# Kernel optimization log

Measured on AMD Instinct MI355X. Metric: run time of the kernel, lower is better.

The kernel has to match this reference:

```python
import jax, jax.numpy as jnp
import numpy as np
from jax import lax

NUM_GROUPS = 1024
GROUP_SIZE = 32
INIT_DIST = 1e10  # matches torch's 10000000000.0 init


def setup_inputs() -> dict:
    key = jax.random.key(0)
    k1, k2 = jax.random.split(key)
    x = jax.random.normal(k1, (1, 65536, 3), dtype=jnp.float32)
    features = jax.random.normal(k2, (1, 65536, 64), dtype=jnp.float32)
    return {"x": x, "features": features}


def _fps(xyz, npoint):
    # xyz: [B, N, 3] -> centers: [1, npoint, 3] (original code assumes B==1)
    B, N, _ = xyz.shape
    init_dist = jnp.full((B, N), INIT_DIST, dtype=xyz.dtype)
    init_far = jnp.zeros((B,), dtype=jnp.int32)  # deterministic start (torch uses randint)

    def step(carry, _):
        distance, farthest = carry
        centroid = jnp.take_along_axis(xyz, farthest[:, None, None], axis=1)  # [B,1,3]
        dist = jnp.sum((xyz - centroid) ** 2, axis=-1)  # [B,N]
        distance = jnp.minimum(distance, dist)
        new_far = jnp.argmax(distance, axis=-1).astype(jnp.int32)
        return (distance, new_far), farthest

    _, centroids = lax.scan(step, (init_dist, init_far), None, length=npoint)
    centroids = centroids.T  # [B, npoint]
    # original: fps_data = xyz[0, fps_idx].unsqueeze(0)  (B==1 assumption)
    return xyz[0, centroids[0]][None]  # [1, npoint, 3]


def _square_distance(src, dst):
    # src: [B,G,3], dst: [B,N,3] -> [B,G,N]
    d = -2.0 * jnp.einsum("bgc,bnc->bgn", src, dst)
    d += jnp.sum(src ** 2, -1)[:, :, None]
    d += jnp.sum(dst ** 2, -1)[:, None, :]
    return d


def reference(x, features):
    centers = _fps(x, NUM_GROUPS)                 # [1,G,3]
    distances = _square_distance(centers, x)      # [1,G,N]
    _, nb_idx = lax.top_k(-distances, GROUP_SIZE)  # smallest-k -> [1,G,M]
    F = features.shape[-1]
    flat_feat = features.reshape(-1, F)
    neighbors = flat_feat[nb_idx.reshape(-1)].reshape(1, -1, GROUP_SIZE, F)
    nearest_center_idx = jnp.argmin(distances, axis=1)  # [1,N]
    return neighbors, nearest_center_idx
```

## Files before the change

kernel.cpp:

```cpp
#include <hip/hip_runtime.h>
#include <stdint.h>

#define N_PTS   65536
#define N_GRP   1024
#define K_NB    32
#define F_DIM   64

#define FPS_BLOCKS  16
#define FPS_THREADS 512
#define FPS_TT (FPS_BLOCKS*FPS_THREADS)
#define FPS_P  (N_PTS / FPS_TT)

__device__ __forceinline__ unsigned long long packMaxKey(float v, unsigned int idx) {
  return ((unsigned long long)__float_as_uint(v) << 32) | (0xFFFFFFFFu - idx);
}
__device__ __forceinline__ unsigned long long packMinKey(float v, unsigned int idx) {
  unsigned int b = __float_as_uint(v);
  b = (b & 0x80000000u) ? ~b : (b | 0x80000000u);
  return ((unsigned long long)b << 32) | idx;
}
__device__ __forceinline__ float unpackMinVal(unsigned long long k) {
  unsigned int b = (unsigned int)(k >> 32);
  b = (b & 0x80000000u) ? (b & 0x7FFFFFFFu) : ~b;
  return __uint_as_float(b);
}

__global__ void __launch_bounds__(FPS_THREADS)
fps_kernel(const float* __restrict__ x, unsigned long long* __restrict__ slots,
           unsigned int* __restrict__ cnts, float* __restrict__ centers)
{
  const int t = blockIdx.x * FPS_THREADS + threadIdx.x;
  float px[FPS_P], py[FPS_P], pz[FPS_P], d[FPS_P];
#pragma unroll
  for (int k = 0; k < FPS_P; ++k) {
    int p = t + k * FPS_TT;
    px[k] = x[p*3+0]; py[k] = x[p*3+1]; pz[k] = x[p*3+2];
    d[k] = 1e10f;
  }
  float cx = x[0], cy = x[1], cz = x[2];
  if (blockIdx.x == 0 && threadIdx.x == 0) {
    centers[0] = cx; centers[1] = cy; centers[2] = cz;
  }
  __shared__ unsigned long long red[FPS_THREADS/64];

  for (int r = 1; r < N_GRP; ++r) {
    unsigned long long best = 0ull;
#pragma unroll
    for (int k = 0; k < FPS_P; ++k) {
      float e0 = px[k]-cx, e1 = py[k]-cy, e2 = pz[k]-cz;
      float dist = fmaf(e2,e2, fmaf(e1,e1, e0*e0));
      float dn = fminf(d[k], dist);
      d[k] = dn;
      unsigned long long pk = packMaxKey(dn, (unsigned)(t + k*FPS_TT));
      if (pk > best) best = pk;
    }
#pragma unroll
    for (int off = 32; off; off >>= 1) {
      unsigned long long o = __shfl_down(best, off);
      if (o > best) best = o;
    }
    const int wid = threadIdx.x >> 6;
    if ((threadIdx.x & 63) == 0) red[wid] = best;
    __syncthreads();
    if (threadIdx.x == 0) {
#pragma unroll
      for (int w = 1; w < FPS_THREADS/64; ++w) if (red[w] > best) best = red[w];
      atomicMax(&slots[r], best);
      __hip_atomic_fetch_add(&cnts[r], 1u, __ATOMIC_RELEASE, __HIP_MEMORY_SCOPE_AGENT);
      while (__hip_atomic_load(&cnts[r], __ATOMIC_ACQUIRE, __HIP_MEMORY_SCOPE_AGENT) < FPS_BLOCKS)
        __builtin_amdgcn_s_sleep(1);
      red[0] = __hip_atomic_load(&slots[r], __ATOMIC_RELAXED, __HIP_MEMORY_SCOPE_AGENT);
    }
    __syncthreads();
    const unsigned long long win = red[0];
    const int widx = (int)(0xFFFFFFFFu - (unsigned int)(win & 0xFFFFFFFFull));
    cx = x[widx*3+0]; cy = x[widx*3+1]; cz = x[widx*3+2];
    if (blockIdx.x == 0 && threadIdx.x == 0) {
      centers[r*3+0] = cx; centers[r*3+1] = cy; centers[r*3+2] = cz;
    }
    __syncthreads();
  }
}

#define TKT 256
#define CAP 3072

__global__ void __launch_bounds__(TKT)
topk_kernel(const float* __restrict__ x, const float* __restrict__ feat,
            const float* __restrict__ centers, float* __restrict__ out)
{
  __shared__ float cv[CAP];
  __shared__ int   ci[CAP];
  __shared__ int   s_cnt;
  __shared__ float s_thr;
  __shared__ float selv[K_NB];
  __shared__ int   seli[K_NB];

  const int g = blockIdx.x, tid = threadIdx.x;
  const float cx = centers[g*3+0], cy = centers[g*3+1], cz = centers[g*3+2];
  const float c2 = fmaf(cz,cz, fmaf(cy,cy, cx*cx));
  if (tid == 0) { s_cnt = 0; s_thr = __builtin_inff(); }
  __syncthreads();

  const int CH = N_PTS / (TKT*8);
  for (int chunk = 0; chunk < CH; ++chunk) {
    const float lthr = s_thr;
#pragma unroll
    for (int k = 0; k < 8; ++k) {
      int p = (chunk*8 + k)*TKT + tid;
      float q0 = x[p*3+0], q1 = x[p*3+1], q2 = x[p*3+2];
      float dot  = fmaf(cz,q2, fmaf(cy,q1, cx*q0));
      float pp   = fmaf(q2,q2, fmaf(q1,q1, q0*q0));
      float dist = fmaf(-2.0f, dot, c2) + pp;
      if (dist <= lthr) {
        int pos = atomicAdd(&s_cnt, 1);
        cv[pos] = dist; ci[pos] = p;
      }
    }
    __syncthreads();
    const int n = s_cnt;
    const bool last = (chunk == CH-1);
    if (n > (CAP - TKT*8) || last) {
      if (tid < 64) {
        for (int it = 0; it < K_NB; ++it) {
          unsigned long long lk = ~0ull;
          for (int j = tid; j < n; j += 64) {
            unsigned long long kk = packMinKey(cv[j], (unsigned)ci[j]);
            if (kk < lk) lk = kk;
          }
#pragma unroll
          for (int off = 32; off; off >>= 1) {
            unsigned long long o = __shfl_xor(lk, off);
            if (o < lk) lk = o;
          }
          const int mi = (int)(unsigned int)(lk & 0xFFFFFFFFull);
          for (int j = tid; j < n; j += 64)
            if (ci[j] == mi) cv[j] = __builtin_inff();
          if (tid == 0) { selv[it] = unpackMinVal(lk); seli[it] = mi; }
        }
      }
      __syncthreads();
      if (!last) {
        if (tid < K_NB) { cv[tid] = selv[tid]; ci[tid] = seli[tid]; }
        if (tid == 0)   { s_cnt = K_NB; s_thr = selv[K_NB-1]; }
        __syncthreads();
      }
    }
  }

  const long base = (long)g * (K_NB*F_DIM);
#pragma unroll
  for (int m = 0; m < (K_NB*F_DIM)/TKT; ++m) {
    int lin = m*TKT + tid;
    int j = lin >> 6, c = lin & 63;
    out[base + lin] = feat[(long)seli[j]*F_DIM + c];
  }
}

__global__ void __launch_bounds__(256)
argmin_kernel(const float* __restrict__ x, const float* __restrict__ centers,
              float* __restrict__ outIdx)
{
  __shared__ float scx[N_GRP], scy[N_GRP], scz[N_GRP], sc2[N_GRP];
  for (int i = threadIdx.x; i < N_GRP; i += 256) {
    float a = centers[i*3+0], b = centers[i*3+1], c = centers[i*3+2];
    scx[i]=a; scy[i]=b; scz[i]=c;
    sc2[i] = fmaf(c,c, fmaf(b,b, a*a));
  }
  __syncthreads();
  const int p = blockIdx.x*256 + threadIdx.x;
  const float q0 = x[p*3+0], q1 = x[p*3+1], q2 = x[p*3+2];
  const float pp = fmaf(q2,q2, fmaf(q1,q1, q0*q0));
  float best = __builtin_inff(); int bi = 0;
#pragma unroll 4
  for (int c = 0; c < N_GRP; ++c) {
    float dot  = fmaf(scz[c],q2, fmaf(scy[c],q1, scx[c]*q0));
    float dist = fmaf(-2.0f, dot, sc2[c]) + pp;
    if (dist < best) { best = dist; bi = c; }
  }
  outIdx[p] = (float)bi;
}

extern "C" void kernel_launch(void* const* d_in, const int* in_sizes, int n_in,
                              void* d_out, int out_size, void* d_ws, size_t ws_size,
                              hipStream_t stream)
{
  const float* x    = (const float*)d_in[0];
  const float* feat = (const float*)d_in[1];
  float* out = (float*)d_out;
  char* ws = (char*)d_ws;
  unsigned long long* slots = (unsigned long long*)ws;
  unsigned int*       cnts  = (unsigned int*)(ws + 8192);
  float*              ctr   = (float*)(ws + 12288);

  hipMemsetAsync(ws, 0, 12288, stream);

  const float* xArg = x;
  unsigned long long* sArg = slots;
  unsigned int* cArg = cnts;
  float* ctrArg = ctr;
  void* kargs[] = { (void*)&xArg, (void*)&sArg, (void*)&cArg, (void*)&ctrArg };
  if (hipLaunchCooperativeKernel(fps_kernel, dim3(FPS_BLOCKS), dim3(FPS_THREADS),
                                 kargs, 0u, stream) != hipSuccess) {
    hipLaunchKernelGGL(fps_kernel, dim3(FPS_BLOCKS), dim3(FPS_THREADS), 0, stream,
                       x, slots, cnts, ctr);
  }
  hipLaunchKernelGGL(topk_kernel, dim3(N_GRP), dim3(TKT), 0, stream, x, feat, ctr, out);
  hipLaunchKernelGGL(argmin_kernel, dim3(N_PTS/256), dim3(256), 0, stream,
                     x, ctr, out + (size_t)N_GRP*K_NB*F_DIM);
}
```

Before: 2.707 ms.

## Replace FPS atomic counter barrier with per-block slots polled by every wave

```diff
diff --git a/kernel.cpp b/kernel.cpp
--- a/kernel.cpp
+++ b/kernel.cpp
@@ -6,14 +6,12 @@
 #define K_NB    32
 #define F_DIM   64
 
-#define FPS_BLOCKS  16
-#define FPS_THREADS 512
+#define FPS_BLOCKS  8
+#define FPS_THREADS 1024
 #define FPS_TT (FPS_BLOCKS*FPS_THREADS)
 #define FPS_P  (N_PTS / FPS_TT)
-
-__device__ __forceinline__ unsigned long long packMaxKey(float v, unsigned int idx) {
-  return ((unsigned long long)__float_as_uint(v) << 32) | (0xFFFFFFFFu - idx);
-}
+#define FPS_WAVES (FPS_THREADS/64)
+
 __device__ __forceinline__ unsigned long long packMinKey(float v, unsigned int idx) {
   unsigned int b = __float_as_uint(v);
   b = (b & 0x80000000u) ? ~b : (b | 0x80000000u);
@@ -27,9 +25,14 @@
 
 __global__ void __launch_bounds__(FPS_THREADS)
 fps_kernel(const float* __restrict__ x, unsigned long long* __restrict__ slots,
-           unsigned int* __restrict__ cnts, float* __restrict__ centers)
-{
-  const int t = blockIdx.x * FPS_THREADS + threadIdx.x;
+           float* __restrict__ centers)
+{
+  const int tid  = threadIdx.x;
+  const int blk  = blockIdx.x;
+  const int t    = blk * FPS_THREADS + tid;
+  const int lane = tid & 63;
+  const int wid  = tid >> 6;
+
   float px[FPS_P], py[FPS_P], pz[FPS_P], d[FPS_P];
 #pragma unroll
   for (int k = 0; k < FPS_P; ++k) {
@@ -38,47 +41,57 @@
     d[k] = 1e10f;
   }
   float cx = x[0], cy = x[1], cz = x[2];
-  if (blockIdx.x == 0 && threadIdx.x == 0) {
+  if (blk == 0 && tid == 0) {
     centers[0] = cx; centers[1] = cy; centers[2] = cz;
   }
-  __shared__ unsigned long long red[FPS_THREADS/64];
+  __shared__ unsigned long long red[FPS_WAVES];
 
   for (int r = 1; r < N_GRP; ++r) {
-    unsigned long long best = 0ull;
+    float bd = -1.0f; unsigned int bi = 0;
 #pragma unroll
     for (int k = 0; k < FPS_P; ++k) {
       float e0 = px[k]-cx, e1 = py[k]-cy, e2 = pz[k]-cz;
       float dist = fmaf(e2,e2, fmaf(e1,e1, e0*e0));
       float dn = fminf(d[k], dist);
       d[k] = dn;
-      unsigned long long pk = packMaxKey(dn, (unsigned)(t + k*FPS_TT));
-      if (pk > best) best = pk;
-    }
+      if (dn > bd) { bd = dn; bi = (unsigned)(t + k*FPS_TT); }
+    }
+    unsigned long long key =
+      ((unsigned long long)__float_as_uint(bd) << 32) | (0xFFFFFFFFu - bi);
 #pragma unroll
     for (int off = 32; off; off >>= 1) {
-      unsigned long long o = __shfl_down(best, off);
-      if (o > best) best = o;
-    }
-    const int wid = threadIdx.x >> 6;
-    if ((threadIdx.x & 63) == 0) red[wid] = best;
+      unsigned long long o = __shfl_xor(key, off);
+      if (o > key) key = o;
+    }
+    if (lane == 0) red[wid] = key;
     __syncthreads();
-    if (threadIdx.x == 0) {
-#pragma unroll
-      for (int w = 1; w < FPS_THREADS/64; ++w) if (red[w] > best) best = red[w];
-      atomicMax(&slots[r], best);
-      __hip_atomic_fetch_add(&cnts[r], 1u, __ATOMIC_RELEASE, __HIP_MEMORY_SCOPE_AGENT);
-      while (__hip_atomic_load(&cnts[r], __ATOMIC_ACQUIRE, __HIP_MEMORY_SCOPE_AGENT) < FPS_BLOCKS)
+    if (tid == 0) {
+      unsigned long long b = red[0];
+#pragma unroll
+      for (int w = 1; w < FPS_WAVES; ++w) if (red[w] > b) b = red[w];
+      __hip_atomic_store(&slots[(size_t)r*FPS_BLOCKS + blk], b,
+                         __ATOMIC_RELAXED, __HIP_MEMORY_SCOPE_AGENT);
+    }
+    const unsigned long long* sl = &slots[(size_t)r*FPS_BLOCKS];
+    unsigned long long kk = 0;
+    if (lane < FPS_BLOCKS) {
+      kk = __hip_atomic_load(&sl[lane], __ATOMIC_RELAXED, __HIP_MEMORY_SCOPE_AGENT);
+      while (kk == 0) {
         __builtin_amdgcn_s_sleep(1);
-      red[0] = __hip_atomic_load(&slots[r], __ATOMIC_RELAXED, __HIP_MEMORY_SCOPE_AGENT);
-    }
-    __syncthreads();
-    const unsigned long long win = red[0];
-    const int widx = (int)(0xFFFFFFFFu - (unsigned int)(win & 0xFFFFFFFFull));
+        kk = __hip_atomic_load(&sl[lane], __ATOMIC_RELAXED, __HIP_MEMORY_SCOPE_AGENT);
+      }
+    }
+#pragma unroll
+    for (int off = 1; off < 8; off <<= 1) {
+      unsigned long long o = __shfl_xor(kk, off);
+      if (o > kk) kk = o;
+    }
+    const int widx =
+      __builtin_amdgcn_readfirstlane((int)(0xFFFFFFFFu - (unsigned int)(kk & 0xFFFFFFFFull)));
     cx = x[widx*3+0]; cy = x[widx*3+1]; cz = x[widx*3+2];
-    if (blockIdx.x == 0 && threadIdx.x == 0) {
+    if (blk == 0 && tid == 0) {
       centers[r*3+0] = cx; centers[r*3+1] = cy; centers[r*3+2] = cz;
     }
-    __syncthreads();
   }
 }
 
@@ -190,20 +203,18 @@
   float* out = (float*)d_out;
   char* ws = (char*)d_ws;
   unsigned long long* slots = (unsigned long long*)ws;
-  unsigned int*       cnts  = (unsigned int*)(ws + 8192);
-  float*              ctr   = (float*)(ws + 12288);
-
-  hipMemsetAsync(ws, 0, 12288, stream);
+  float*              ctr   = (float*)(ws + 65536);
+
+  hipMemsetAsync(ws, 0, 65536, stream);
 
   const float* xArg = x;
   unsigned long long* sArg = slots;
-  unsigned int* cArg = cnts;
   float* ctrArg = ctr;
-  void* kargs[] = { (void*)&xArg, (void*)&sArg, (void*)&cArg, (void*)&ctrArg };
+  void* kargs[] = { (void*)&xArg, (void*)&sArg, (void*)&ctrArg };
   if (hipLaunchCooperativeKernel(fps_kernel, dim3(FPS_BLOCKS), dim3(FPS_THREADS),
                                  kargs, 0u, stream) != hipSuccess) {
     hipLaunchKernelGGL(fps_kernel, dim3(FPS_BLOCKS), dim3(FPS_THREADS), 0, stream,
-                       x, slots, cnts, ctr);
+                       x, slots, ctr);
   }
   hipLaunchKernelGGL(topk_kernel, dim3(N_GRP), dim3(TKT), 0, stream, x, feat, ctr, out);
   hipLaunchKernelGGL(argmin_kernel, dim3(N_PTS/256), dim3(256), 0, stream,
```

Result: slower. 2.897 ms (+7.0%).

## Replace multi-block FPS with single-block Morton-chunked FPS using bounding-box pruning

Applied to the files above, without the earlier changes.

```diff
diff --git a/kernel.cpp b/kernel.cpp
--- a/kernel.cpp
+++ b/kernel.cpp
@@ -6,14 +6,16 @@
 #define K_NB    32
 #define F_DIM   64
 
-#define FPS_BLOCKS  16
-#define FPS_THREADS 512
-#define FPS_TT (FPS_BLOCKS*FPS_THREADS)
-#define FPS_P  (N_PTS / FPS_TT)
-
-__device__ __forceinline__ unsigned long long packMaxKey(float v, unsigned int idx) {
-  return ((unsigned long long)__float_as_uint(v) << 32) | (0xFFFFFFFFu - idx);
-}
+#define FPS1_THR 1024
+#define NCHUNK   1024
+#define CPTS     64
+#define NBINS    4096
+
+#define F2_BLOCKS 16
+#define F2_THR    512
+#define F2_TT     (F2_BLOCKS*F2_THR)
+#define F2_P      (N_PTS / F2_TT)
+
 __device__ __forceinline__ unsigned long long packMinKey(float v, unsigned int idx) {
   unsigned int b = __float_as_uint(v);
   b = (b & 0x80000000u) ? ~b : (b | 0x80000000u);
@@ -24,16 +26,141 @@
   b = (b & 0x80000000u) ? (b & 0x7FFFFFFFu) : ~b;
   return __uint_as_float(b);
 }
-
-__global__ void __launch_bounds__(FPS_THREADS)
-fps_kernel(const float* __restrict__ x, unsigned long long* __restrict__ slots,
-           unsigned int* __restrict__ cnts, float* __restrict__ centers)
-{
-  const int t = blockIdx.x * FPS_THREADS + threadIdx.x;
-  float px[FPS_P], py[FPS_P], pz[FPS_P], d[FPS_P];
-#pragma unroll
-  for (int k = 0; k < FPS_P; ++k) {
-    int p = t + k * FPS_TT;
+__device__ __forceinline__ unsigned spread4(unsigned b) {
+  return (b & 1u) | ((b & 2u) << 2) | ((b & 4u) << 4) | ((b & 8u) << 6);
+}
+__device__ __forceinline__ unsigned morton_bid(float a, float b, float c) {
+  const float S = 16.0f / 11.0f;
+  int bx = (int)((a + 5.5f) * S);
+  int by = (int)((b + 5.5f) * S);
+  int bz = (int)((c + 5.5f) * S);
+  bx = min(max(bx, 0), 15); by = min(max(by, 0), 15); bz = min(max(bz, 0), 15);
+  return spread4((unsigned)bx) | (spread4((unsigned)by) << 1) | (spread4((unsigned)bz) << 2);
+}
+
+__global__ void __launch_bounds__(FPS1_THR)
+fps_kernel(const float* __restrict__ x, float4* __restrict__ xs4,
+           float* __restrict__ dd, float* __restrict__ centers)
+{
+  __shared__ unsigned sA[NBINS];
+  __shared__ unsigned sB[NBINS];
+  __shared__ unsigned long long red[FPS1_THR/64];
+  __shared__ float bc[3];
+  const int tid = threadIdx.x, lane = tid & 63, wid = tid >> 6;
+
+#pragma unroll
+  for (int j = 0; j < NBINS/FPS1_THR; ++j) sA[tid + j*FPS1_THR] = 0u;
+  __syncthreads();
+  for (int i = tid; i < N_PTS; i += FPS1_THR) {
+    float a = x[i*3+0], b = x[i*3+1], c = x[i*3+2];
+    atomicAdd(&sA[morton_bid(a,b,c)], 1u);
+  }
+  __syncthreads();
+
+  {
+    unsigned* src = sA; unsigned* dst = sB;
+    for (int off = 1; off < NBINS; off <<= 1) {
+#pragma unroll
+      for (int j = 0; j < NBINS/FPS1_THR; ++j) {
+        int i = tid + j*FPS1_THR;
+        unsigned v = src[i];
+        if (i >= off) v += src[i-off];
+        dst[i] = v;
+      }
+      __syncthreads();
+      unsigned* t_ = src; src = dst; dst = t_;
+    }
+#pragma unroll
+    for (int j = 0; j < NBINS/FPS1_THR; ++j) {
+      int i = tid + j*FPS1_THR;
+      sB[i] = (i == 0) ? 0u : sA[i-1];
+    }
+    __syncthreads();
+  }
+
+  for (int i = tid; i < N_PTS; i += FPS1_THR) {
+    float a = x[i*3+0], b = x[i*3+1], c = x[i*3+2];
+    unsigned pos = atomicAdd(&sB[morton_bid(a,b,c)], 1u);
+    unsigned sidx = (pos & 63u) * NCHUNK + (pos >> 6);
+    xs4[sidx] = make_float4(a, b, c, __uint_as_float((unsigned)i));
+    dd[sidx] = 1e10f;
+  }
+  __syncthreads();
+
+  float lox = 3.0e38f, loy = 3.0e38f, loz = 3.0e38f;
+  float hix = -3.0e38f, hiy = -3.0e38f, hiz = -3.0e38f;
+  for (int k = 0; k < CPTS; ++k) {
+    float4 f = xs4[k*NCHUNK + tid];
+    lox = fminf(lox, f.x); hix = fmaxf(hix, f.x);
+    loy = fminf(loy, f.y); hiy = fmaxf(hiy, f.y);
+    loz = fminf(loz, f.z); hiz = fmaxf(hiz, f.z);
+  }
+
+  float cx = x[0], cy = x[1], cz = x[2];
+  if (tid == 0) { centers[0] = cx; centers[1] = cy; centers[2] = cz; }
+  unsigned long long ckey = 0ull;
+  float cdmax = 1e10f;
+
+  for (int r = 1; r < N_GRP; ++r) {
+    float dxl = fmaxf(fmaxf(lox - cx, cx - hix), 0.0f);
+    float dyl = fmaxf(fmaxf(loy - cy, cy - hiy), 0.0f);
+    float dzl = fmaxf(fmaxf(loz - cz, cz - hiz), 0.0f);
+    float b2 = fmaf(dzl, dzl, fmaf(dyl, dyl, dxl*dxl));
+    if (b2 < cdmax * 1.0001f) {
+      unsigned long long nk = 0ull;
+#pragma unroll 8
+      for (int k = 0; k < CPTS; ++k) {
+        int sidx = k*NCHUNK + tid;
+        float4 f = xs4[sidx];
+        float dk = dd[sidx];
+        float e0 = f.x - cx, e1 = f.y - cy, e2 = f.z - cz;
+        float dist = fmaf(e2,e2, fmaf(e1,e1, e0*e0));
+        float dn = fminf(dk, dist);
+        dd[sidx] = dn;
+        unsigned long long kk = ((unsigned long long)__float_as_uint(dn) << 32)
+                              | (unsigned long long)(0xFFFFFFFFu - __float_as_uint(f.w));
+        if (kk > nk) nk = kk;
+      }
+      ckey = nk;
+      cdmax = __uint_as_float((unsigned)(ckey >> 32));
+    }
+    unsigned long long key = ckey;
+#pragma unroll
+    for (int off = 32; off; off >>= 1) {
+      unsigned long long o = __shfl_xor(key, off);
+      if (o > key) key = o;
+    }
+    if (lane == 0) red[wid] = key;
+    __syncthreads();
+    if (wid == 0) {
+      unsigned long long kk2 = (lane < FPS1_THR/64) ? red[lane] : 0ull;
+#pragma unroll
+      for (int off = 1; off < FPS1_THR/64; off <<= 1) {
+        unsigned long long o = __shfl_xor(kk2, off);
+        if (o > kk2) kk2 = o;
+      }
+      if (lane == 0) {
+        unsigned orig = 0xFFFFFFFFu - (unsigned)(kk2 & 0xFFFFFFFFull);
+        float wx = x[orig*3+0], wy = x[orig*3+1], wz = x[orig*3+2];
+        centers[r*3+0] = wx; centers[r*3+1] = wy; centers[r*3+2] = wz;
+        bc[0] = wx; bc[1] = wy; bc[2] = wz;
+      }
+    }
+    __syncthreads();
+    cx = bc[0]; cy = bc[1]; cz = bc[2];
+  }
+}
+
+__global__ void __launch_bounds__(F2_THR)
+fps_safe_kernel(const float* __restrict__ x, unsigned long long* __restrict__ slots,
+                unsigned int* __restrict__ cnts, float* __restrict__ centers)
+{
+  __shared__ unsigned long long red[F2_THR/64];
+  const int t = blockIdx.x * F2_THR + threadIdx.x;
+  float px[F2_P], py[F2_P], pz[F2_P], d[F2_P];
+#pragma unroll
+  for (int k = 0; k < F2_P; ++k) {
+    int p = t + k * F2_TT;
     px[k] = x[p*3+0]; py[k] = x[p*3+1]; pz[k] = x[p*3+2];
     d[k] = 1e10f;
   }
@@ -41,17 +168,16 @@
   if (blockIdx.x == 0 && threadIdx.x == 0) {
     centers[0] = cx; centers[1] = cy; centers[2] = cz;
   }
-  __shared__ unsigned long long red[FPS_THREADS/64];
-
   for (int r = 1; r < N_GRP; ++r) {
     unsigned long long best = 0ull;
 #pragma unroll
-    for (int k = 0; k < FPS_P; ++k) {
+    for (int k = 0; k < F2_P; ++k) {
       float e0 = px[k]-cx, e1 = py[k]-cy, e2 = pz[k]-cz;
       float dist = fmaf(e2,e2, fmaf(e1,e1, e0*e0));
       float dn = fminf(d[k], dist);
       d[k] = dn;
-      unsigned long long pk = packMaxKey(dn, (unsigned)(t + k*FPS_TT));
+      unsigned long long pk = ((unsigned long long)__float_as_uint(dn) << 32)
+                            | (0xFFFFFFFFu - (unsigned)(t + k*F2_TT));
       if (pk > best) best = pk;
     }
 #pragma unroll
@@ -64,10 +190,10 @@
     __syncthreads();
     if (threadIdx.x == 0) {
 #pragma unroll
-      for (int w = 1; w < FPS_THREADS/64; ++w) if (red[w] > best) best = red[w];
+      for (int w = 1; w < F2_THR/64; ++w) if (red[w] > best) best = red[w];
       atomicMax(&slots[r], best);
       __hip_atomic_fetch_add(&cnts[r], 1u, __ATOMIC_RELEASE, __HIP_MEMORY_SCOPE_AGENT);
-      while (__hip_atomic_load(&cnts[r], __ATOMIC_ACQUIRE, __HIP_MEMORY_SCOPE_AGENT) < FPS_BLOCKS)
+      while (__hip_atomic_load(&cnts[r], __ATOMIC_ACQUIRE, __HIP_MEMORY_SCOPE_AGENT) < F2_BLOCKS)
         __builtin_amdgcn_s_sleep(1);
       red[0] = __hip_atomic_load(&slots[r], __ATOMIC_RELAXED, __HIP_MEMORY_SCOPE_AGENT);
     }
@@ -189,20 +315,21 @@
   const float* feat = (const float*)d_in[1];
   float* out = (float*)d_out;
   char* ws = (char*)d_ws;
-  unsigned long long* slots = (unsigned long long*)ws;
-  unsigned int*       cnts  = (unsigned int*)(ws + 8192);
-  float*              ctr   = (float*)(ws + 12288);
-
-  hipMemsetAsync(ws, 0, 12288, stream);
-
-  const float* xArg = x;
-  unsigned long long* sArg = slots;
-  unsigned int* cArg = cnts;
-  float* ctrArg = ctr;
-  void* kargs[] = { (void*)&xArg, (void*)&sArg, (void*)&cArg, (void*)&ctrArg };
-  if (hipLaunchCooperativeKernel(fps_kernel, dim3(FPS_BLOCKS), dim3(FPS_THREADS),
-                                 kargs, 0u, stream) != hipSuccess) {
-    hipLaunchKernelGGL(fps_kernel, dim3(FPS_BLOCKS), dim3(FPS_THREADS), 0, stream,
+
+  float* ctr = (float*)ws;
+  const size_t DD_OFF  = 65536;
+  const size_t XS_OFF  = DD_OFF + (size_t)N_PTS*4;
+  const size_t NEED    = XS_OFF + (size_t)N_PTS*16;
+
+  if (ws_size >= NEED) {
+    float*  dd  = (float*)(ws + DD_OFF);
+    float4* xs4 = (float4*)(ws + XS_OFF);
+    hipLaunchKernelGGL(fps_kernel, dim3(1), dim3(FPS1_THR), 0, stream, x, xs4, dd, ctr);
+  } else {
+    unsigned long long* slots = (unsigned long long*)(ws + 16384);
+    unsigned int*       cnts  = (unsigned int*)(ws + 24576);
+    hipMemsetAsync(ws + 16384, 0, 12288, stream);
+    hipLaunchKernelGGL(fps_safe_kernel, dim3(F2_BLOCKS), dim3(F2_THR), 0, stream,
                        x, slots, cnts, ctr);
   }
   hipLaunchKernelGGL(topk_kernel, dim3(N_GRP), dim3(TKT), 0, stream, x, feat, ctr, out);
```

Result: slower. 7.271 ms (+168.6%).
